# Optimization experiments

Measured on AMD Instinct MI355X. Metric: run time of the kernel, lower is better.

The kernel has to match this reference:

```python
import jax, jax.numpy as jnp
import numpy as np

CLAMP_LO, CLAMP_HI, CLAMP_GATE_MAX = -10.0, 10.0, 10.0
E, TOPK = 8, 2
M, K, N = 2048, 2048, 1408  # tokens, hidden_dim, intermediate_dim
CAPACITY = 2 * (M * TOPK // E)


def setup_inputs() -> dict:
    key = jax.random.key(0)
    ks = jax.random.split(key, 6)
    bk = 1.0 / np.sqrt(K)  # kaiming_uniform(a=sqrt(5)) bound = 1/sqrt(fan_in)
    bn = 1.0 / np.sqrt(N)
    return {
        "flat_h": jax.random.normal(ks[0], (M, K), jnp.float32),
        "flat_idx": jax.random.randint(ks[1], (M, TOPK), 0, E),
        "flat_gate": jax.random.uniform(ks[2], (M, TOPK), jnp.float32),
        "gate_weight": jax.random.uniform(ks[3], (E, N, K), jnp.float32, -bk, bk),
        "up_weight": jax.random.uniform(ks[4], (E, N, K), jnp.float32, -bk, bk),
        "down_weight": jax.random.uniform(ks[5], (E, K, N), jnp.float32, -bn, bn),
    }


def reference(flat_h, flat_idx, flat_gate, gate_weight, up_weight, down_weight):
    m, top_k = flat_idx.shape
    k = flat_h.shape[1]
    e = gate_weight.shape[0]
    r = m * top_k

    expert_id = flat_idx.reshape(-1)                                   # (R,)
    gate = flat_gate.reshape(-1)                                       # (R,)
    token_index = jnp.repeat(jnp.arange(m, dtype=jnp.int32), top_k)    # (R,)

    # stable sort rows by expert id (mirrors torch.argsort(..., stable=True))
    sort_idx = jnp.argsort(expert_id, stable=True)
    sorted_eid = expert_id[sort_idx]
    tok_sorted = token_index[sort_idx]
    gate_sorted = gate[sort_idx]

    # position of each sorted row inside its expert group
    counts = jnp.bincount(expert_id, length=e)
    starts = jnp.concatenate([jnp.zeros(1, counts.dtype), jnp.cumsum(counts)[:-1]])
    pos = jnp.arange(r) - starts[sorted_eid]                           # (R,)

    # dispatch: scatter sorted tokens into fixed-capacity (E, C, K) buffer
    buf = jnp.zeros((e, CAPACITY, k), flat_h.dtype)
    buf = buf.at[sorted_eid, pos].set(flat_h[tok_sorted])

    # grouped GEMMs: weights stored (E, out, in) like nn.Linear
    g = jnp.einsum("eck,enk->ecn", buf, gate_weight)
    g = jnp.minimum(g, CLAMP_GATE_MAX)
    u = jnp.clip(jnp.einsum("eck,enk->ecn", buf, up_weight), CLAMP_LO, CLAMP_HI)
    h = jax.nn.silu(g) * u                                             # SwiGLU (E, C, N)
    d = jnp.einsum("ecn,ekn->eck", h, down_weight)                     # (E, C, K)

    # combine: gather each routed row back, weight by gate, sum over top_k slots
    expert_out = d[sorted_eid, pos]                                    # (R, K)
    weighted = expert_out * gate_sorted[:, None]
    out = jnp.zeros((m, k), flat_h.dtype).at[tok_sorted].add(weighted)
    return out
```

## Files before the change

kernel.cpp:

```cpp
#include <hip/hip_runtime.h>

#define M_TOK 2048
#define KDIM 2048
#define NDIM 1408
#define NEXP 8
#define RROWS (M_TOK * 2)
#define CAP 1024

typedef __attribute__((ext_vector_type(8))) short short8;
typedef __attribute__((ext_vector_type(4))) float f32x4;

__device__ __forceinline__ unsigned short bf16rn(float f) {
    unsigned int u = __builtin_bit_cast(unsigned int, f);
    u += 0x7FFFu + ((u >> 16) & 1u);
    return (unsigned short)(u >> 16);
}
__device__ __forceinline__ unsigned int pk2(float a, float b) {
    return (unsigned int)bf16rn(a) | ((unsigned int)bf16rn(b) << 16);
}

__global__ void k_route(const float* __restrict__ h, const int* __restrict__ idx,
                        const float* __restrict__ gate, int* __restrict__ cnt,
                        int* __restrict__ tok_of, float* __restrict__ gate_of,
                        unsigned short* __restrict__ bufA) {
    int r = blockIdx.x;
    __shared__ int s_ep;
    if (threadIdx.x == 0) {
        int e = idx[r];
        int p = atomicAdd(&cnt[e], 1);
        tok_of[e * CAP + p] = r >> 1;
        gate_of[e * CAP + p] = gate[r];
        s_ep = e * CAP + p;
    }
    __syncthreads();
    int ep = s_ep;
    const float4* src = (const float4*)(h + (size_t)(r >> 1) * KDIM) + threadIdx.x * 2;
    float4 a = src[0], b = src[1];
    uint4 o;
    o.x = pk2(a.x, a.y); o.y = pk2(a.z, a.w);
    o.z = pk2(b.x, b.y); o.w = pk2(b.z, b.w);
    *((uint4*)(bufA + (size_t)ep * KDIM) + threadIdx.x) = o;
}

__global__ __launch_bounds__(256, 2)
void k_gemm1(const unsigned short* __restrict__ bufA,
             const float* __restrict__ gw, const float* __restrict__ uw,
             const int* __restrict__ cnt, unsigned short* __restrict__ hbuf) {
    const int e = blockIdx.z;
    const int m0 = blockIdx.y * 128;
    if (m0 >= cnt[e]) return;
    const int n0 = blockIdx.x * 128;

    const unsigned short* A = bufA + (size_t)e * CAP * KDIM;
    const float* Bg = gw + (size_t)e * NDIM * KDIM;
    const float* Bu = uw + (size_t)e * NDIM * KDIM;

    __shared__ unsigned short sA[128 * 40];
    __shared__ unsigned short sG[128 * 40];
    __shared__ unsigned short sU[128 * 40];

    const int tid = threadIdx.x;
    const int lane = tid & 63;
    const int wave = tid >> 6;
    const int wm = (wave >> 1) * 64, wn = (wave & 1) * 64;
    const int q = lane >> 4, l15 = lane & 15;

    f32x4 accG[4][4] = {};
    f32x4 accU[4][4] = {};

    for (int k0 = 0; k0 < KDIM; k0 += 32) {
        __syncthreads();
#pragma unroll
        for (int g = 0; g < 2; g++) {
            int gg = tid + g * 256;
            int row = gg >> 2, c8 = (gg & 3) * 8;
            *(uint4*)&sA[row * 40 + c8] =
                *(const uint4*)(A + (size_t)(m0 + row) * KDIM + k0 + c8);
        }
#pragma unroll
        for (int g = 0; g < 2; g++) {
            int gg = tid + g * 256;
            int row = gg >> 2, c8 = (gg & 3) * 8;
            const float4* pg = (const float4*)(Bg + (size_t)(n0 + row) * KDIM + k0 + c8);
            float4 a = pg[0], b = pg[1];
            uint4 o;
            o.x = pk2(a.x, a.y); o.y = pk2(a.z, a.w);
            o.z = pk2(b.x, b.y); o.w = pk2(b.z, b.w);
            *(uint4*)&sG[row * 40 + c8] = o;
            const float4* pu = (const float4*)(Bu + (size_t)(n0 + row) * KDIM + k0 + c8);
            a = pu[0]; b = pu[1];
            o.x = pk2(a.x, a.y); o.y = pk2(a.z, a.w);
            o.z = pk2(b.x, b.y); o.w = pk2(b.z, b.w);
            *(uint4*)&sU[row * 40 + c8] = o;
        }
        __syncthreads();

        short8 af[4], gf[4], uf[4];
#pragma unroll
        for (int i = 0; i < 4; i++) {
            af[i] = *(const short8*)&sA[(wm + i * 16 + l15) * 40 + q * 8];
            gf[i] = *(const short8*)&sG[(wn + i * 16 + l15) * 40 + q * 8];
            uf[i] = *(const short8*)&sU[(wn + i * 16 + l15) * 40 + q * 8];
        }
#pragma unroll
        for (int i = 0; i < 4; i++)
#pragma unroll
            for (int j = 0; j < 4; j++) {
                accG[i][j] = __builtin_amdgcn_mfma_f32_16x16x32_bf16(af[i], gf[j], accG[i][j], 0, 0, 0);
                accU[i][j] = __builtin_amdgcn_mfma_f32_16x16x32_bf16(af[i], uf[j], accU[i][j], 0, 0, 0);
            }
    }

    unsigned short* H = hbuf + (size_t)e * CAP * NDIM;
#pragma unroll
    for (int i = 0; i < 4; i++)
#pragma unroll
        for (int j = 0; j < 4; j++) {
            int col = n0 + wn + j * 16 + l15;
#pragma unroll
            for (int rg = 0; rg < 4; rg++) {
                int row = m0 + wm + i * 16 + q * 4 + rg;
                float g = accG[i][j][rg];
                float u = accU[i][j][rg];
                g = fminf(g, 10.f);
                u = fminf(fmaxf(u, -10.f), 10.f);
                float hv = g / (1.f + __expf(-g)) * u;
                H[(size_t)row * NDIM + col] = bf16rn(hv);
            }
        }
}

__global__ __launch_bounds__(256, 2)
void k_gemm2(const unsigned short* __restrict__ hbuf,
             const float* __restrict__ dw, const int* __restrict__ cnt,
             const int* __restrict__ tok_of, const float* __restrict__ gate_of,
             float* __restrict__ out) {
    const int e = blockIdx.z;
    const int cnt_e = cnt[e];
    const int m0 = blockIdx.y * 128;
    if (m0 >= cnt_e) return;
    const int n0 = blockIdx.x * 128;

    const unsigned short* A = hbuf + (size_t)e * CAP * NDIM;
    const float* B = dw + (size_t)e * KDIM * NDIM;

    __shared__ unsigned short sA[128 * 40];
    __shared__ unsigned short sB[128 * 40];

    const int tid = threadIdx.x;
    const int lane = tid & 63;
    const int wave = tid >> 6;
    const int wm = (wave >> 1) * 64, wn = (wave & 1) * 64;
    const int q = lane >> 4, l15 = lane & 15;

    f32x4 acc[4][4] = {};

    for (int k0 = 0; k0 < NDIM; k0 += 32) {
        __syncthreads();
#pragma unroll
        for (int g = 0; g < 2; g++) {
            int gg = tid + g * 256;
            int row = gg >> 2, c8 = (gg & 3) * 8;
            *(uint4*)&sA[row * 40 + c8] =
                *(const uint4*)(A + (size_t)(m0 + row) * NDIM + k0 + c8);
        }
#pragma unroll
        for (int g = 0; g < 2; g++) {
            int gg = tid + g * 256;
            int row = gg >> 2, c8 = (gg & 3) * 8;
            const float4* pb = (const float4*)(B + (size_t)(n0 + row) * NDIM + k0 + c8);
            float4 a = pb[0], b = pb[1];
            uint4 o;
            o.x = pk2(a.x, a.y); o.y = pk2(a.z, a.w);
            o.z = pk2(b.x, b.y); o.w = pk2(b.z, b.w);
            *(uint4*)&sB[row * 40 + c8] = o;
        }
        __syncthreads();

        short8 af[4], bfr[4];
#pragma unroll
        for (int i = 0; i < 4; i++) {
            af[i] = *(const short8*)&sA[(wm + i * 16 + l15) * 40 + q * 8];
            bfr[i] = *(const short8*)&sB[(wn + i * 16 + l15) * 40 + q * 8];
        }
#pragma unroll
        for (int i = 0; i < 4; i++)
#pragma unroll
            for (int j = 0; j < 4; j++)
                acc[i][j] = __builtin_amdgcn_mfma_f32_16x16x32_bf16(af[i], bfr[j], acc[i][j], 0, 0, 0);
    }

#pragma unroll
    for (int i = 0; i < 4; i++) {
#pragma unroll
        for (int rg = 0; rg < 4; rg++) {
            int row = m0 + wm + i * 16 + q * 4 + rg;
            if (row < cnt_e) {
                int tok = tok_of[e * CAP + row];
                float gt = gate_of[e * CAP + row];
                float* orow = out + (size_t)tok * KDIM + n0 + wn + l15;
#pragma unroll
                for (int j = 0; j < 4; j++)
                    atomicAdd(orow + j * 16, acc[i][j][rg] * gt);
            }
        }
    }
}

extern "C" void kernel_launch(void* const* d_in, const int* in_sizes, int n_in,
                              void* d_out, int out_size, void* d_ws, size_t ws_size,
                              hipStream_t stream) {
    const float* flat_h = (const float*)d_in[0];
    const int* flat_idx = (const int*)d_in[1];
    const float* flat_gate = (const float*)d_in[2];
    const float* gw = (const float*)d_in[3];
    const float* uw = (const float*)d_in[4];
    const float* dwn = (const float*)d_in[5];
    float* out = (float*)d_out;

    char* w = (char*)d_ws;
    int* cnt = (int*)w;
    int* tok_of = (int*)(w + 256);
    float* gate_of = (float*)(w + 256 + NEXP * CAP * 4);
    unsigned short* bufA = (unsigned short*)(w + 256 + 2 * NEXP * CAP * 4);
    unsigned short* hbuf = (unsigned short*)(w + 256 + 2 * NEXP * CAP * 4 +
                                             (size_t)NEXP * CAP * KDIM * 2);

    hipMemsetAsync(cnt, 0, 256, stream);
    hipMemsetAsync(out, 0, (size_t)M_TOK * KDIM * 4, stream);

    k_route<<<RROWS, 256, 0, stream>>>(flat_h, flat_idx, flat_gate, cnt, tok_of, gate_of, bufA);
    k_gemm1<<<dim3(NDIM / 128, CAP / 128, NEXP), 256, 0, stream>>>(bufA, gw, uw, cnt, hbuf);
    k_gemm2<<<dim3(KDIM / 128, CAP / 128, NEXP), 256, 0, stream>>>(hbuf, dwn, cnt, tok_of, gate_of, out);
}
```

Baseline: 512.6 us.

## Pre-convert expert weights to bf16 and stage GEMM tiles via direct global-to-LDS loads

Adds a conversion kernel that turns gate, up and down weights into bf16 once per call, so both GEMMs read bf16 weights instead of converting fp32 tiles inside every block. The tile loads now use global_load_lds to write straight into unpadded shared memory, with no trip through registers. The goal is less register pressure and less conversion work repeated across the M tiles. The cost is an extra full pass over all weights each call (read fp32, write bf16) and possible LDS bank conflicts, since the row padding is gone.

```diff
diff --git a/kernel.cpp b/kernel.cpp
--- a/kernel.cpp
+++ b/kernel.cpp
@@ -17,6 +17,12 @@
 }
 __device__ __forceinline__ unsigned int pk2(float a, float b) {
     return (unsigned int)bf16rn(a) | ((unsigned int)bf16rn(b) << 16);
+}
+
+__device__ __forceinline__ void glds16(const void* g, void* l) {
+    __builtin_amdgcn_global_load_lds(
+        (const __attribute__((address_space(1))) unsigned int*)g,
+        (__attribute__((address_space(3))) unsigned int*)l, 16, 0, 0);
 }
 
 __global__ void k_route(const float* __restrict__ h, const int* __restrict__ idx,
@@ -42,9 +48,20 @@
     *((uint4*)(bufA + (size_t)ep * KDIM) + threadIdx.x) = o;
 }
 
+__global__ void k_cvt(const float* __restrict__ src, unsigned short* __restrict__ dst) {
+    int i = blockIdx.x * blockDim.x + threadIdx.x;
+    const float4* s = (const float4*)src + (size_t)i * 2;
+    float4 a = s[0], b = s[1];
+    uint4 o;
+    o.x = pk2(a.x, a.y); o.y = pk2(a.z, a.w);
+    o.z = pk2(b.x, b.y); o.w = pk2(b.z, b.w);
+    ((uint4*)dst)[i] = o;
+}
+
 __global__ __launch_bounds__(256, 2)
 void k_gemm1(const unsigned short* __restrict__ bufA,
-             const float* __restrict__ gw, const float* __restrict__ uw,
+             const unsigned short* __restrict__ gwb,
+             const unsigned short* __restrict__ uwb,
              const int* __restrict__ cnt, unsigned short* __restrict__ hbuf) {
     const int e = blockIdx.z;
     const int m0 = blockIdx.y * 128;
@@ -52,18 +69,20 @@
     const int n0 = blockIdx.x * 128;
 
     const unsigned short* A = bufA + (size_t)e * CAP * KDIM;
-    const float* Bg = gw + (size_t)e * NDIM * KDIM;
-    const float* Bu = uw + (size_t)e * NDIM * KDIM;
-
-    __shared__ unsigned short sA[128 * 40];
-    __shared__ unsigned short sG[128 * 40];
-    __shared__ unsigned short sU[128 * 40];
+    const unsigned short* G = gwb + (size_t)e * NDIM * KDIM;
+    const unsigned short* U = uwb + (size_t)e * NDIM * KDIM;
+
+    __shared__ unsigned short sA[128 * 32];
+    __shared__ unsigned short sG[128 * 32];
+    __shared__ unsigned short sU[128 * 32];
 
     const int tid = threadIdx.x;
     const int lane = tid & 63;
     const int wave = tid >> 6;
     const int wm = (wave >> 1) * 64, wn = (wave & 1) * 64;
     const int q = lane >> 4, l15 = lane & 15;
+    const int r4 = lane >> 2, c8 = (lane & 3) * 8;
+    const int seg0 = wave * 2;
 
     f32x4 accG[4][4] = {};
     f32x4 accU[4][4] = {};
@@ -71,36 +90,21 @@
     for (int k0 = 0; k0 < KDIM; k0 += 32) {
         __syncthreads();
 #pragma unroll
-        for (int g = 0; g < 2; g++) {
-            int gg = tid + g * 256;
-            int row = gg >> 2, c8 = (gg & 3) * 8;
-            *(uint4*)&sA[row * 40 + c8] =
-                *(const uint4*)(A + (size_t)(m0 + row) * KDIM + k0 + c8);
-        }
-#pragma unroll
-        for (int g = 0; g < 2; g++) {
-            int gg = tid + g * 256;
-            int row = gg >> 2, c8 = (gg & 3) * 8;
-            const float4* pg = (const float4*)(Bg + (size_t)(n0 + row) * KDIM + k0 + c8);
-            float4 a = pg[0], b = pg[1];
-            uint4 o;
-            o.x = pk2(a.x, a.y); o.y = pk2(a.z, a.w);
-            o.z = pk2(b.x, b.y); o.w = pk2(b.z, b.w);
-            *(uint4*)&sG[row * 40 + c8] = o;
-            const float4* pu = (const float4*)(Bu + (size_t)(n0 + row) * KDIM + k0 + c8);
-            a = pu[0]; b = pu[1];
-            o.x = pk2(a.x, a.y); o.y = pk2(a.z, a.w);
-            o.z = pk2(b.x, b.y); o.w = pk2(b.z, b.w);
-            *(uint4*)&sU[row * 40 + c8] = o;
+        for (int c = 0; c < 2; c++) {
+            int seg = seg0 + c;
+            int row = seg * 16 + r4;
+            glds16(A + (size_t)(m0 + row) * KDIM + k0 + c8, &sA[seg * 512]);
+            glds16(G + (size_t)(n0 + row) * KDIM + k0 + c8, &sG[seg * 512]);
+            glds16(U + (size_t)(n0 + row) * KDIM + k0 + c8, &sU[seg * 512]);
         }
         __syncthreads();
 
         short8 af[4], gf[4], uf[4];
 #pragma unroll
         for (int i = 0; i < 4; i++) {
-            af[i] = *(const short8*)&sA[(wm + i * 16 + l15) * 40 + q * 8];
-            gf[i] = *(const short8*)&sG[(wn + i * 16 + l15) * 40 + q * 8];
-            uf[i] = *(const short8*)&sU[(wn + i * 16 + l15) * 40 + q * 8];
+            af[i] = *(const short8*)&sA[(wm + i * 16 + l15) * 32 + q * 8];
+            gf[i] = *(const short8*)&sG[(wn + i * 16 + l15) * 32 + q * 8];
+            uf[i] = *(const short8*)&sU[(wn + i * 16 + l15) * 32 + q * 8];
         }
 #pragma unroll
         for (int i = 0; i < 4; i++)
@@ -132,7 +136,7 @@
 
 __global__ __launch_bounds__(256, 2)
 void k_gemm2(const unsigned short* __restrict__ hbuf,
-             const float* __restrict__ dw, const int* __restrict__ cnt,
+             const unsigned short* __restrict__ dwb, const int* __restrict__ cnt,
              const int* __restrict__ tok_of, const float* __restrict__ gate_of,
              float* __restrict__ out) {
     const int e = blockIdx.z;
@@ -142,46 +146,37 @@
     const int n0 = blockIdx.x * 128;
 
     const unsigned short* A = hbuf + (size_t)e * CAP * NDIM;
-    const float* B = dw + (size_t)e * KDIM * NDIM;
-
-    __shared__ unsigned short sA[128 * 40];
-    __shared__ unsigned short sB[128 * 40];
+    const unsigned short* B = dwb + (size_t)e * KDIM * NDIM;
+
+    __shared__ unsigned short sA[128 * 32];
+    __shared__ unsigned short sB[128 * 32];
 
     const int tid = threadIdx.x;
     const int lane = tid & 63;
     const int wave = tid >> 6;
     const int wm = (wave >> 1) * 64, wn = (wave & 1) * 64;
     const int q = lane >> 4, l15 = lane & 15;
+    const int r4 = lane >> 2, c8 = (lane & 3) * 8;
+    const int seg0 = wave * 2;
 
     f32x4 acc[4][4] = {};
 
     for (int k0 = 0; k0 < NDIM; k0 += 32) {
         __syncthreads();
 #pragma unroll
-        for (int g = 0; g < 2; g++) {
-            int gg = tid + g * 256;
-            int row = gg >> 2, c8 = (gg & 3) * 8;
-            *(uint4*)&sA[row * 40 + c8] =
-                *(const uint4*)(A + (size_t)(m0 + row) * NDIM + k0 + c8);
-        }
-#pragma unroll
-        for (int g = 0; g < 2; g++) {
-            int gg = tid + g * 256;
-            int row = gg >> 2, c8 = (gg & 3) * 8;
-            const float4* pb = (const float4*)(B + (size_t)(n0 + row) * NDIM + k0 + c8);
-            float4 a = pb[0], b = pb[1];
-            uint4 o;
-            o.x = pk2(a.x, a.y); o.y = pk2(a.z, a.w);
-            o.z = pk2(b.x, b.y); o.w = pk2(b.z, b.w);
-            *(uint4*)&sB[row * 40 + c8] = o;
+        for (int c = 0; c < 2; c++) {
+            int seg = seg0 + c;
+            int row = seg * 16 + r4;
+            glds16(A + (size_t)(m0 + row) * NDIM + k0 + c8, &sA[seg * 512]);
+            glds16(B + (size_t)(n0 + row) * NDIM + k0 + c8, &sB[seg * 512]);
         }
         __syncthreads();
 
         short8 af[4], bfr[4];
 #pragma unroll
         for (int i = 0; i < 4; i++) {
-            af[i] = *(const short8*)&sA[(wm + i * 16 + l15) * 40 + q * 8];
-            bfr[i] = *(const short8*)&sB[(wn + i * 16 + l15) * 40 + q * 8];
+            af[i] = *(const short8*)&sA[(wm + i * 16 + l15) * 32 + q * 8];
+            bfr[i] = *(const short8*)&sB[(wn + i * 16 + l15) * 32 + q * 8];
         }
 #pragma unroll
         for (int i = 0; i < 4; i++)
@@ -222,14 +217,21 @@
     int* cnt = (int*)w;
     int* tok_of = (int*)(w + 256);
     float* gate_of = (float*)(w + 256 + NEXP * CAP * 4);
-    unsigned short* bufA = (unsigned short*)(w + 256 + 2 * NEXP * CAP * 4);
-    unsigned short* hbuf = (unsigned short*)(w + 256 + 2 * NEXP * CAP * 4 +
-                                             (size_t)NEXP * CAP * KDIM * 2);
+    unsigned short* bufA = (unsigned short*)(w + (1ull << 20));
+    unsigned short* hbuf = (unsigned short*)(w + (33ull << 20));
+    unsigned short* gwb  = (unsigned short*)(w + (56ull << 20));
+    unsigned short* uwb  = (unsigned short*)(w + (100ull << 20));
+    unsigned short* dwb  = (unsigned short*)(w + (144ull << 20));
 
     hipMemsetAsync(cnt, 0, 256, stream);
     hipMemsetAsync(out, 0, (size_t)M_TOK * KDIM * 4, stream);
 
+    const int welems8 = NEXP * NDIM * KDIM / 8;
+    k_cvt<<<welems8 / 256, 256, 0, stream>>>(gw, gwb);
+    k_cvt<<<welems8 / 256, 256, 0, stream>>>(uw, uwb);
+    k_cvt<<<welems8 / 256, 256, 0, stream>>>(dwn, dwb);
+
     k_route<<<RROWS, 256, 0, stream>>>(flat_h, flat_idx, flat_gate, cnt, tok_of, gate_of, bufA);
-    k_gemm1<<<dim3(NDIM / 128, CAP / 128, NEXP), 256, 0, stream>>>(bufA, gw, uw, cnt, hbuf);
-    k_gemm2<<<dim3(KDIM / 128, CAP / 128, NEXP), 256, 0, stream>>>(hbuf, dwn, cnt, tok_of, gate_of, out);
-}
+    k_gemm1<<<dim3(NDIM / 128, CAP / 128, NEXP), 256, 0, stream>>>(bufA, gwb, uwb, cnt, hbuf);
+    k_gemm2<<<dim3(KDIM / 128, CAP / 128, NEXP), 256, 0, stream>>>(hbuf, dwb, cnt, tok_of, gate_of, out);
+}
```

Result: no change. 518.7 us (+1.2%).
